# Performance work log

Hardware: AMD Instinct MI355X
Metric: run time of the kernel (lower is better)

The kernel has to match this reference:

```python
import jax, jax.numpy as jnp
import numpy as np

N_NODES = 100000
N_EDGES = 1_600_000
D_IN, D_H, D_L = 128, 64, 32


def setup_inputs() -> dict:
    key = jax.random.key(0)
    ks = jax.random.split(key, 12)
    def w(k, fi, fo):
        return jax.random.normal(k, (fi, fo), dtype=jnp.float32) * (1.0 / np.sqrt(fi))
    return {
        "x": jax.random.normal(ks[0], (N_NODES, D_IN), dtype=jnp.float32),
        "edge_index": jax.random.randint(ks[1], (2, N_EDGES), 0, N_NODES, dtype=jnp.int32),
        "W1": w(ks[2], D_IN, D_H), "b1": jnp.zeros((D_H,), jnp.float32),
        "W2": w(ks[3], D_H, D_H), "b2": jnp.zeros((D_H,), jnp.float32),
        "Wmu": w(ks[4], D_H, D_L), "bmu": jnp.zeros((D_L,), jnp.float32),
        "Wlv": w(ks[5], D_H, D_L), "blv": jnp.zeros((D_L,), jnp.float32),
    }


def _gcn_conv(x, W, b, src, dst, dis):
    # PyG GCNConv: x' = D^{-1/2} (A + I) D^{-1/2} (x W) + b
    h = x @ W                                   # (N, out) -- transform first (out <= in)
    norm = dis[src] * dis[dst]                  # (E,) symmetric normalization
    agg = jax.ops.segment_sum(h[src] * norm[:, None], dst, num_segments=x.shape[0])
    agg = agg + h * (dis * dis)[:, None]        # self-loop contribution
    return agg + b


def reference(x, edge_index, W1, b1, W2, b2, Wmu, bmu, Wlv, blv):
    N = x.shape[0]
    src, dst = edge_index[0], edge_index[1]
    # degree of A + I (count incoming edges at dst, plus self loop)
    deg = jax.ops.segment_sum(jnp.ones(src.shape, x.dtype), dst, num_segments=N) + 1.0
    dis = jax.lax.rsqrt(deg)                    # deg^{-1/2}
    h = jax.nn.relu(_gcn_conv(x, W1, b1, src, dst, dis))
    # dropout is identity at inference
    h = jax.nn.relu(_gcn_conv(h, W2, b2, src, dst, dis))
    mu = _gcn_conv(h, Wmu, bmu, src, dst, dis)
    logvar = _gcn_conv(h, Wlv, blv, src, dst, dis)
    return (mu, logvar)
```

## Files before the change

kernel.cpp:

```cpp
#include <hip/hip_runtime.h>
#include <hip/hip_fp16.h>


#define B1 256

__global__ __launch_bounds__(256) void histk_kernel(const int* __restrict__ dst,
                                                    int* __restrict__ hist2,
                                                    int E, int K, int chunk) {
  __shared__ int h[1024];
  for (int i = threadIdx.x; i < K; i += 256) h[i] = 0;
  __syncthreads();
  const int e0 = blockIdx.x * chunk;
  const int e1 = min(E, e0 + chunk);
  for (int e = e0 + threadIdx.x; e < e1; e += 256)
    atomicAdd(&h[dst[e] >> 7], 1);
  __syncthreads();
  for (int i = threadIdx.x; i < K; i += 256)
    hist2[i * B1 + blockIdx.x] = h[i];
}

__global__ __launch_bounds__(256) void scanA_kernel(const int* __restrict__ cnt,
                                                    int* __restrict__ excl,
                                                    int* __restrict__ bsum, int M) {
  __shared__ int sm[256];
  const int tid = threadIdx.x;
  const int i = blockIdx.x * 256 + tid;
  int v = (i < M) ? cnt[i] : 0;
  sm[tid] = v;
  __syncthreads();
#pragma unroll
  for (int off = 1; off < 256; off <<= 1) {
    int t = (tid >= off) ? sm[tid - off] : 0;
    __syncthreads();
    sm[tid] += t;
    __syncthreads();
  }
  if (i < M) excl[i] = sm[tid] - v;
  if (tid == 255) bsum[blockIdx.x] = sm[255];
}

__global__ __launch_bounds__(1024) void scanB_kernel(int* __restrict__ bsum, int nb) {
  __shared__ int sm[1024];
  const int tid = threadIdx.x;
  int v = (tid < nb) ? bsum[tid] : 0;
  sm[tid] = v;
  __syncthreads();
#pragma unroll
  for (int off = 1; off < 1024; off <<= 1) {
    int t = (tid >= off) ? sm[tid - off] : 0;
    __syncthreads();
    sm[tid] += t;
    __syncthreads();
  }
  if (tid < nb) bsum[tid] = sm[tid] - v;
}

__global__ __launch_bounds__(256) void scanC_kernel(int* __restrict__ data,
                                                    const int* __restrict__ bsum, int M) {
  int i = blockIdx.x * 256 + threadIdx.x;
  if (i < M) data[i] += bsum[i >> 8];
}

__global__ __launch_bounds__(256) void scat1_kernel(const int* __restrict__ src,
                                                    const int* __restrict__ dst,
                                                    const int* __restrict__ off2,
                                                    int* __restrict__ ebuf,
                                                    int E, int K, int chunk) {
  __shared__ int base[1024];
  __shared__ int cur[1024];
  for (int i = threadIdx.x; i < K; i += 256) {
    base[i] = off2[i * B1 + blockIdx.x];
    cur[i] = 0;
  }
  __syncthreads();
  const int e0 = blockIdx.x * chunk;
  const int e1 = min(E, e0 + chunk);
  for (int e = e0 + threadIdx.x; e < e1; e += 256) {
    int d = dst[e];
    int k = d >> 7;
    int p = base[k] + atomicAdd(&cur[k], 1);
    ebuf[p] = ((d & 127) << 17) | src[e];
  }
}

__global__ __launch_bounds__(256) void bsort_kernel(const int* __restrict__ ebuf,
                                                    const int* __restrict__ off2,
                                                    int* __restrict__ esrc,
                                                    int* __restrict__ rowptr,
                                                    float* __restrict__ dis,
                                                    int N, int E, int K) {
  const int k = blockIdx.x;
  const int tid = threadIdx.x;
  const int s0 = off2[k * B1];
  const int s1 = (k + 1 < K) ? off2[(k + 1) * B1] : E;
  const int cnt = s1 - s0;
  __shared__ int sm[128];
  __shared__ int rexcl[128];
  __shared__ int rcur[128];
  if (tid < 128) sm[tid] = 0;
  __syncthreads();
  for (int i = tid; i < cnt; i += 256)
    atomicAdd(&sm[ebuf[s0 + i] >> 17], 1);
  __syncthreads();
  int myc = (tid < 128) ? sm[tid] : 0;
#pragma unroll
  for (int off = 1; off < 128; off <<= 1) {
    int t = (tid >= off && tid < 128) ? sm[tid - off] : 0;
    __syncthreads();
    if (tid < 128) sm[tid] += t;
    __syncthreads();
  }
  if (tid < 128) {
    int ex = sm[tid] - myc;
    rexcl[tid] = ex;
    rcur[tid] = 0;
    int row = (k << 7) + tid;
    if (row < N) {
      rowptr[row] = s0 + ex;
      dis[row] = rsqrtf((float)myc + 1.0f);
    }
  }
  if (k == K - 1 && tid == 0) rowptr[N] = E;
  __syncthreads();
  for (int i = tid; i < cnt; i += 256) {
    int v = ebuf[s0 + i];
    int r = v >> 17;
    int p = s0 + rexcl[r] + atomicAdd(&rcur[r], 1);
    esrc[p] = v & 0x1FFFF;
  }
}

__global__ __launch_bounds__(256) void packw_kernel(const float* __restrict__ Wmu,
                                                    const float* __restrict__ Wlv,
                                                    float* __restrict__ Wc) {
  int i = blockIdx.x * blockDim.x + threadIdx.x;
  if (i < 64 * 64) {
    int k = i >> 6, c = i & 63;
    Wc[i] = (c < 32) ? Wmu[k * 32 + c] : Wlv[k * 32 + (c - 32)];
  }
}

__global__ __launch_bounds__(256) void gemm64_kernel(const float* __restrict__ X,
                                                     const float* __restrict__ W,
                                                     const float* __restrict__ dis,
                                                     __half* __restrict__ Hs,
                                                     int N, int Din) {
  __shared__ float sA[32][68];
  __shared__ float sB[32][68];
  const int tid = threadIdx.x;
  const int tc = tid & 15;
  const int tr = tid >> 4;
  const int row0 = blockIdx.x * 64;

  float acc[4][4];
#pragma unroll
  for (int i = 0; i < 4; ++i)
#pragma unroll
    for (int j = 0; j < 4; ++j) acc[i][j] = 0.f;

  for (int k0 = 0; k0 < Din; k0 += 32) {
#pragma unroll
    for (int i = tid; i < 64 * 32; i += 256) {
      int r = i >> 5, kk = i & 31;
      int gr = row0 + r;
      sA[kk][r] = (gr < N) ? X[(size_t)gr * Din + k0 + kk] : 0.f;
    }
#pragma unroll
    for (int i = tid; i < 32 * 64; i += 256) {
      int kk = i >> 6, c = i & 63;
      sB[kk][c] = W[(size_t)(k0 + kk) * 64 + c];
    }
    __syncthreads();
#pragma unroll
    for (int kk = 0; kk < 32; ++kk) {
      float4 a = *(const float4*)&sA[kk][tr * 4];
      float4 b = *(const float4*)&sB[kk][tc * 4];
      acc[0][0] += a.x * b.x; acc[0][1] += a.x * b.y; acc[0][2] += a.x * b.z; acc[0][3] += a.x * b.w;
      acc[1][0] += a.y * b.x; acc[1][1] += a.y * b.y; acc[1][2] += a.y * b.z; acc[1][3] += a.y * b.w;
      acc[2][0] += a.z * b.x; acc[2][1] += a.z * b.y; acc[2][2] += a.z * b.z; acc[2][3] += a.z * b.w;
      acc[3][0] += a.w * b.x; acc[3][1] += a.w * b.y; acc[3][2] += a.w * b.z; acc[3][3] += a.w * b.w;
    }
    __syncthreads();
  }
  unsigned short* hsu = (unsigned short*)Hs;
#pragma unroll
  for (int i = 0; i < 4; ++i) {
    int gr = row0 + tr * 4 + i;
    if (gr < N) {
      float dd = dis[gr];
      ushort4 v;
      v.x = __half_as_ushort(__float2half_rn(acc[i][0] * dd));
      v.y = __half_as_ushort(__float2half_rn(acc[i][1] * dd));
      v.z = __half_as_ushort(__float2half_rn(acc[i][2] * dd));
      v.w = __half_as_ushort(__float2half_rn(acc[i][3] * dd));
      *(ushort4*)&hsu[(size_t)gr * 64 + tc * 4] = v;
    }
  }
}

__global__ __launch_bounds__(256) void agg_fused_kernel(const __half* __restrict__ Hs,
                                                        const int* __restrict__ esrc,
                                                        const int* __restrict__ rowptr,
                                                        const float* __restrict__ dis,
                                                        const float* __restrict__ b,
                                                        float* __restrict__ Y,
                                                        int N, int relu) {
  const int lane = threadIdx.x & 63;
  const int half = lane >> 5;
  const int c = lane & 31;
  const int row = (blockIdx.x * 256 + threadIdx.x) >> 6;
  if (row >= N) return;
  const __half2* __restrict__ Hs2 = (const __half2*)Hs;
  const int k1 = rowptr[row + 1];
  int k = rowptr[row];
  float ax = 0.f, ay = 0.f;
  for (; k + 8 <= k1; k += 8) {
    int s0 = esrc[k + 0 + half];
    int s1 = esrc[k + 2 + half];
    int s2 = esrc[k + 4 + half];
    int s3 = esrc[k + 6 + half];
    float2 f0 = __half22float2(Hs2[(size_t)s0 * 32 + c]);
    float2 f1 = __half22float2(Hs2[(size_t)s1 * 32 + c]);
    float2 f2 = __half22float2(Hs2[(size_t)s2 * 32 + c]);
    float2 f3 = __half22float2(Hs2[(size_t)s3 * 32 + c]);
    ax += f0.x + f1.x + f2.x + f3.x;
    ay += f0.y + f1.y + f2.y + f3.y;
  }
  for (; k < k1; k += 2) {
    int kk = k + half;
    if (kk < k1) {
      float2 f = __half22float2(Hs2[(size_t)esrc[kk] * 32 + c]);
      ax += f.x; ay += f.y;
    }
  }
  ax += __shfl_xor(ax, 32);
  ay += __shfl_xor(ay, 32);
  if (half == 0) {
    float2 sf = __half22float2(Hs2[(size_t)row * 32 + c]);
    float dd = dis[row];
    float vx = dd * (ax + sf.x) + b[2 * c];
    float vy = dd * (ay + sf.y) + b[2 * c + 1];
    if (relu) { vx = fmaxf(vx, 0.f); vy = fmaxf(vy, 0.f); }
    *(float2*)&Y[(size_t)row * 64 + 2 * c] = make_float2(vx, vy);
  }
}

__global__ __launch_bounds__(256) void agg_mulv_kernel(const __half* __restrict__ Hs,
                                                       const int* __restrict__ esrc,
                                                       const int* __restrict__ rowptr,
                                                       const float* __restrict__ dis,
                                                       const float* __restrict__ bmu,
                                                       const float* __restrict__ blv,
                                                       float* __restrict__ out, int N) {
  const int lane = threadIdx.x & 63;
  const int half = lane >> 5;
  const int c = lane & 31;
  const int row = (blockIdx.x * 256 + threadIdx.x) >> 6;
  if (row >= N) return;
  const __half2* __restrict__ Hs2 = (const __half2*)Hs;
  const int k1 = rowptr[row + 1];
  int k = rowptr[row];
  float ax = 0.f, ay = 0.f;
  for (; k + 8 <= k1; k += 8) {
    int s0 = esrc[k + 0 + half];
    int s1 = esrc[k + 2 + half];
    int s2 = esrc[k + 4 + half];
    int s3 = esrc[k + 6 + half];
    float2 f0 = __half22float2(Hs2[(size_t)s0 * 32 + c]);
    float2 f1 = __half22float2(Hs2[(size_t)s1 * 32 + c]);
    float2 f2 = __half22float2(Hs2[(size_t)s2 * 32 + c]);
    float2 f3 = __half22float2(Hs2[(size_t)s3 * 32 + c]);
    ax += f0.x + f1.x + f2.x + f3.x;
    ay += f0.y + f1.y + f2.y + f3.y;
  }
  for (; k < k1; k += 2) {
    int kk = k + half;
    if (kk < k1) {
      float2 f = __half22float2(Hs2[(size_t)esrc[kk] * 32 + c]);
      ax += f.x; ay += f.y;
    }
  }
  ax += __shfl_xor(ax, 32);
  ay += __shfl_xor(ay, 32);
  if (half == 0) {
    float2 sf = __half22float2(Hs2[(size_t)row * 32 + c]);
    float dd = dis[row];
    float vx = dd * (ax + sf.x);
    float vy = dd * (ay + sf.y);
    if (c < 16) {
      vx += bmu[2 * c]; vy += bmu[2 * c + 1];
      *(float2*)&out[(size_t)row * 32 + 2 * c] = make_float2(vx, vy);
    } else {
      int cc = 2 * c - 32;
      vx += blv[cc]; vy += blv[cc + 1];
      *(float2*)&out[(size_t)N * 32 + (size_t)row * 32 + cc] = make_float2(vx, vy);
    }
  }
}

extern "C" void kernel_launch(void* const* d_in, const int* in_sizes, int n_in,
                              void* d_out, int out_size, void* d_ws, size_t ws_size,
                              hipStream_t stream) {
  const float* x   = (const float*)d_in[0];
  const int*   ei  = (const int*)d_in[1];
  const float* W1  = (const float*)d_in[2];
  const float* b1  = (const float*)d_in[3];
  const float* W2  = (const float*)d_in[4];
  const float* b2  = (const float*)d_in[5];
  const float* Wmu = (const float*)d_in[6];
  const float* bmu = (const float*)d_in[7];
  const float* Wlv = (const float*)d_in[8];
  const float* blv = (const float*)d_in[9];

  const int N = in_sizes[0] / 128;
  const int E = in_sizes[1] / 2;
  const int* src = ei;
  const int* dst = ei + E;

  const int K = (N + 127) >> 7;
  const int M = K * B1;
  const int chunk = (E + B1 - 1) / B1;

  const size_t N64 = (size_t)N * 64;
  __half* Hs    = (__half*)d_ws;
  float* YBUF   = (float*)(Hs + N64);
  float* dis    = YBUF + N64;
  int*   rowptr = (int*)(dis + N);
  int*   hist2  = rowptr + N + 1;
  int*   bsum   = hist2 + M;
  int*   ebuf   = bsum + 1024;
  int*   esrc   = ebuf + E;
  float* Wc     = (float*)(esrc + E);
  float* out    = (float*)d_out;

  const int rowBlocks = (N * 64 + 255) / 256;
  const int gemmBlocks = (N + 63) / 64;

  histk_kernel<<<B1, 256, 0, stream>>>(dst, hist2, E, K, chunk);
  scanA_kernel<<<K, 256, 0, stream>>>(hist2, hist2, bsum, M);
  scanB_kernel<<<1, 1024, 0, stream>>>(bsum, K);
  scanC_kernel<<<K, 256, 0, stream>>>(hist2, bsum, M);
  scat1_kernel<<<B1, 256, 0, stream>>>(src, dst, hist2, ebuf, E, K, chunk);
  bsort_kernel<<<K, 256, 0, stream>>>(ebuf, hist2, esrc, rowptr, dis, N, E, K);
  packw_kernel<<<16, 256, 0, stream>>>(Wmu, Wlv, Wc);

  gemm64_kernel<<<gemmBlocks, 256, 0, stream>>>(x, W1, dis, Hs, N, 128);
  agg_fused_kernel<<<rowBlocks, 256, 0, stream>>>(Hs, esrc, rowptr, dis, b1, YBUF, N, 1);

  gemm64_kernel<<<gemmBlocks, 256, 0, stream>>>(YBUF, W2, dis, Hs, N, 64);
  agg_fused_kernel<<<rowBlocks, 256, 0, stream>>>(Hs, esrc, rowptr, dis, b2, YBUF, N, 1);

  gemm64_kernel<<<gemmBlocks, 256, 0, stream>>>(YBUF, Wc, dis, Hs, N, 64);
  agg_mulv_kernel<<<rowBlocks, 256, 0, stream>>>(Hs, esrc, rowptr, dis, bmu, blv, out, N);
}
```

Measured before the change: 426.1 us.

## Use fp16 MFMA GEMMs with pre-transposed weights and fp16 intermediate activations

Replaces the scalar FP32 tiled GEMM with a 16x16x32 fp16 MFMA kernel. Weights are pre-transposed and padded into fp16 in LDS, and the A operands are read straight from global memory. The aggregation kernels now write the hidden activations as fp16, which halves the intermediate store and reload traffic for the next GEMM. The cost is extra fp16 rounding on the inputs, weights and hidden activations. The output stores are also scattered per element rather than vectorised.

```diff
diff --git a/kernel.cpp b/kernel.cpp
--- a/kernel.cpp
+++ b/kernel.cpp
@@ -3,6 +3,9 @@
 
 
 #define B1 256
+
+typedef _Float16 f16x8 __attribute__((ext_vector_type(8)));
+typedef float f32x4 __attribute__((ext_vector_type(4)));
 
 __global__ __launch_bounds__(256) void histk_kernel(const int* __restrict__ dst,
                                                     int* __restrict__ hist2,
@@ -130,70 +133,81 @@
   }
 }
 
-__global__ __launch_bounds__(256) void packw_kernel(const float* __restrict__ Wmu,
-                                                    const float* __restrict__ Wlv,
-                                                    float* __restrict__ Wc) {
-  int i = blockIdx.x * blockDim.x + threadIdx.x;
-  if (i < 64 * 64) {
-    int k = i >> 6, c = i & 63;
-    Wc[i] = (c < 32) ? Wmu[k * 32 + c] : Wlv[k * 32 + (c - 32)];
-  }
-}
-
-__global__ __launch_bounds__(256) void gemm64_kernel(const float* __restrict__ X,
-                                                     const float* __restrict__ W,
-                                                     const float* __restrict__ dis,
-                                                     __half* __restrict__ Hs,
-                                                     int N, int Din) {
-  __shared__ float sA[32][68];
-  __shared__ float sB[32][68];
+__global__ __launch_bounds__(256) void packwT_kernel(const float* __restrict__ W1,
+                                                     const float* __restrict__ W2,
+                                                     const float* __restrict__ Wmu,
+                                                     const float* __restrict__ Wlv,
+                                                     __half* __restrict__ W1t,
+                                                     __half* __restrict__ W2t,
+                                                     __half* __restrict__ Wct) {
+  int i = blockIdx.x * 256 + threadIdx.x;
+  if (i < 64 * 136) {
+    int c = i / 136, k = i % 136;
+    W1t[i] = (k < 128) ? __float2half_rn(W1[k * 64 + c]) : __float2half_rn(0.f);
+  }
+  if (i < 64 * 72) {
+    int c = i / 72, k = i % 72;
+    W2t[i] = (k < 64) ? __float2half_rn(W2[k * 64 + c]) : __float2half_rn(0.f);
+    float wc = 0.f;
+    if (k < 64) wc = (c < 32) ? Wmu[k * 32 + c] : Wlv[k * 32 + (c - 32)];
+    Wct[i] = __float2half_rn(wc);
+  }
+}
+
+template <int DIN, bool F32IN>
+__global__ __launch_bounds__(256) void gemm_mfma_kernel(const void* __restrict__ Xin,
+                                                        const __half* __restrict__ Wt,
+                                                        const float* __restrict__ dis,
+                                                        __half* __restrict__ Hs, int N) {
+  constexpr int KP = DIN + 8;
+  __shared__ __half sW[64 * KP];
   const int tid = threadIdx.x;
-  const int tc = tid & 15;
-  const int tr = tid >> 4;
-  const int row0 = blockIdx.x * 64;
-
-  float acc[4][4];
-#pragma unroll
-  for (int i = 0; i < 4; ++i)
-#pragma unroll
-    for (int j = 0; j < 4; ++j) acc[i][j] = 0.f;
-
-  for (int k0 = 0; k0 < Din; k0 += 32) {
-#pragma unroll
-    for (int i = tid; i < 64 * 32; i += 256) {
-      int r = i >> 5, kk = i & 31;
-      int gr = row0 + r;
-      sA[kk][r] = (gr < N) ? X[(size_t)gr * Din + k0 + kk] : 0.f;
-    }
-#pragma unroll
-    for (int i = tid; i < 32 * 64; i += 256) {
-      int kk = i >> 6, c = i & 63;
-      sB[kk][c] = W[(size_t)(k0 + kk) * 64 + c];
-    }
-    __syncthreads();
-#pragma unroll
-    for (int kk = 0; kk < 32; ++kk) {
-      float4 a = *(const float4*)&sA[kk][tr * 4];
-      float4 b = *(const float4*)&sB[kk][tc * 4];
-      acc[0][0] += a.x * b.x; acc[0][1] += a.x * b.y; acc[0][2] += a.x * b.z; acc[0][3] += a.x * b.w;
-      acc[1][0] += a.y * b.x; acc[1][1] += a.y * b.y; acc[1][2] += a.y * b.z; acc[1][3] += a.y * b.w;
-      acc[2][0] += a.z * b.x; acc[2][1] += a.z * b.y; acc[2][2] += a.z * b.z; acc[2][3] += a.z * b.w;
-      acc[3][0] += a.w * b.x; acc[3][1] += a.w * b.y; acc[3][2] += a.w * b.z; acc[3][3] += a.w * b.w;
-    }
-    __syncthreads();
-  }
-  unsigned short* hsu = (unsigned short*)Hs;
-#pragma unroll
-  for (int i = 0; i < 4; ++i) {
-    int gr = row0 + tr * 4 + i;
-    if (gr < N) {
-      float dd = dis[gr];
-      ushort4 v;
-      v.x = __half_as_ushort(__float2half_rn(acc[i][0] * dd));
-      v.y = __half_as_ushort(__float2half_rn(acc[i][1] * dd));
-      v.z = __half_as_ushort(__float2half_rn(acc[i][2] * dd));
-      v.w = __half_as_ushort(__float2half_rn(acc[i][3] * dd));
-      *(ushort4*)&hsu[(size_t)gr * 64 + tc * 4] = v;
+  for (int i = tid * 8; i < 64 * KP; i += 256 * 8)
+    *(f16x8*)&sW[i] = *(const f16x8*)&Wt[i];
+  __syncthreads();
+
+  const int w = tid >> 6;
+  const int lane = tid & 63;
+  const int r16 = lane & 15;
+  const int kq = lane >> 4;
+  const int nodeA = blockIdx.x * 64 + w * 16 + r16;
+  const int nodeAc = min(nodeA, N - 1);
+
+  f32x4 acc[4];
+#pragma unroll
+  for (int ct = 0; ct < 4; ++ct) acc[ct] = (f32x4){0.f, 0.f, 0.f, 0.f};
+
+#pragma unroll
+  for (int kt = 0; kt < DIN / 32; ++kt) {
+    const int kb = kt * 32 + kq * 8;
+    f16x8 a;
+    if constexpr (F32IN) {
+      const float* X = (const float*)Xin;
+      float4 a0 = *(const float4*)&X[(size_t)nodeAc * DIN + kb];
+      float4 a1 = *(const float4*)&X[(size_t)nodeAc * DIN + kb + 4];
+      a[0] = (_Float16)a0.x; a[1] = (_Float16)a0.y;
+      a[2] = (_Float16)a0.z; a[3] = (_Float16)a0.w;
+      a[4] = (_Float16)a1.x; a[5] = (_Float16)a1.y;
+      a[6] = (_Float16)a1.z; a[7] = (_Float16)a1.w;
+    } else {
+      const __half* X = (const __half*)Xin;
+      a = *(const f16x8*)&X[(size_t)nodeAc * DIN + kb];
+    }
+#pragma unroll
+    for (int ct = 0; ct < 4; ++ct) {
+      f16x8 bf = *(const f16x8*)&sW[(ct * 16 + r16) * KP + kb];
+      acc[ct] = __builtin_amdgcn_mfma_f32_16x16x32_f16(a, bf, acc[ct], 0, 0, 0);
+    }
+  }
+
+#pragma unroll
+  for (int j = 0; j < 4; ++j) {
+    const int orow = blockIdx.x * 64 + w * 16 + kq * 4 + j;
+    if (orow < N) {
+      const float dd = dis[orow];
+#pragma unroll
+      for (int ct = 0; ct < 4; ++ct)
+        Hs[(size_t)orow * 64 + ct * 16 + r16] = __float2half_rn(acc[ct][j] * dd);
     }
   }
 }
@@ -203,7 +217,7 @@
                                                         const int* __restrict__ rowptr,
                                                         const float* __restrict__ dis,
                                                         const float* __restrict__ b,
-                                                        float* __restrict__ Y,
+                                                        __half* __restrict__ Y,
                                                         int N, int relu) {
   const int lane = threadIdx.x & 63;
   const int half = lane >> 5;
@@ -241,7 +255,7 @@
     float vx = dd * (ax + sf.x) + b[2 * c];
     float vy = dd * (ay + sf.y) + b[2 * c + 1];
     if (relu) { vx = fmaxf(vx, 0.f); vy = fmaxf(vy, 0.f); }
-    *(float2*)&Y[(size_t)row * 64 + 2 * c] = make_float2(vx, vy);
+    ((__half2*)Y)[(size_t)row * 32 + c] = __floats2half2_rn(vx, vy);
   }
 }
 
@@ -323,14 +337,16 @@
 
   const size_t N64 = (size_t)N * 64;
   __half* Hs    = (__half*)d_ws;
-  float* YBUF   = (float*)(Hs + N64);
-  float* dis    = YBUF + N64;
+  __half* Yh    = Hs + N64;
+  __half* W1t   = Yh + N64;
+  __half* W2t   = W1t + 64 * 136;
+  __half* Wct   = W2t + 64 * 72;
+  float* dis    = (float*)(Wct + 64 * 72);
   int*   rowptr = (int*)(dis + N);
   int*   hist2  = rowptr + N + 1;
   int*   bsum   = hist2 + M;
   int*   ebuf   = bsum + 1024;
   int*   esrc   = ebuf + E;
-  float* Wc     = (float*)(esrc + E);
   float* out    = (float*)d_out;
 
   const int rowBlocks = (N * 64 + 255) / 256;
@@ -342,14 +358,14 @@
   scanC_kernel<<<K, 256, 0, stream>>>(hist2, bsum, M);
   scat1_kernel<<<B1, 256, 0, stream>>>(src, dst, hist2, ebuf, E, K, chunk);
   bsort_kernel<<<K, 256, 0, stream>>>(ebuf, hist2, esrc, rowptr, dis, N, E, K);
-  packw_kernel<<<16, 256, 0, stream>>>(Wmu, Wlv, Wc);
-
-  gemm64_kernel<<<gemmBlocks, 256, 0, stream>>>(x, W1, dis, Hs, N, 128);
-  agg_fused_kernel<<<rowBlocks, 256, 0, stream>>>(Hs, esrc, rowptr, dis, b1, YBUF, N, 1);
-
-  gemm64_kernel<<<gemmBlocks, 256, 0, stream>>>(YBUF, W2, dis, Hs, N, 64);
-  agg_fused_kernel<<<rowBlocks, 256, 0, stream>>>(Hs, esrc, rowptr, dis, b2, YBUF, N, 1);
-
-  gemm64_kernel<<<gemmBlocks, 256, 0, stream>>>(YBUF, Wc, dis, Hs, N, 64);
+  packwT_kernel<<<34, 256, 0, stream>>>(W1, W2, Wmu, Wlv, W1t, W2t, Wct);
+
+  gemm_mfma_kernel<128, true><<<gemmBlocks, 256, 0, stream>>>(x, W1t, dis, Hs, N);
+  agg_fused_kernel<<<rowBlocks, 256, 0, stream>>>(Hs, esrc, rowptr, dis, b1, Yh, N, 1);
+
+  gemm_mfma_kernel<64, false><<<gemmBlocks, 256, 0, stream>>>(Yh, W2t, dis, Hs, N);
+  agg_fused_kernel<<<rowBlocks, 256, 0, stream>>>(Hs, esrc, rowptr, dis, b2, Yh, N, 1);
+
+  gemm_mfma_kernel<64, false><<<gemmBlocks, 256, 0, stream>>>(Yh, Wct, dis, Hs, N);
   agg_mulv_kernel<<<rowBlocks, 256, 0, stream>>>(Hs, esrc, rowptr, dis, bmu, blv, out, N);
 }
```

Result: faster. 362.2 us (-15.0%).
